# Performance work log

Hardware: AMD Instinct MI355X
Metric: run time of the kernel (lower is better)

The kernel has to match this reference:

```python
import jax, jax.numpy as jnp
import numpy as np
from jax import lax

GAMMA = 1.0
LAM = 1.0
ITERS = 20          # fixed PGD iterations for the graph fused-lasso solve
B = 2048            # number of graphs
NMAX = 1536         # max graph size (for padded per-graph sparsemax)


def setup_inputs() -> dict:
    sizes = (512 + (np.arange(B, dtype=np.int64) * 997) % 1025).astype(np.int32)
    N = int(sizes.sum())  # 2098092
    offsets = np.concatenate([[0], np.cumsum(sizes)[:-1]]).astype(np.int64)
    gid = np.repeat(np.arange(B, dtype=np.int64), sizes)
    # chain edges within each graph
    same = gid[1:] == gid[:-1]
    ca = np.arange(N - 1, dtype=np.int64)[same]
    cb = ca + 1
    # one random intra-graph edge per node
    rng = np.random.RandomState(0)
    u = rng.randint(0, 1 << 30, size=(N, 2)).astype(np.int64)
    ra = offsets[gid] + u[:, 0] % sizes[gid]
    rb = offsets[gid] + u[:, 1] % sizes[gid]
    edges = np.stack([np.concatenate([ca, ra]), np.concatenate([cb, rb])], axis=1).astype(np.int32)
    key = jax.random.key(0)
    x = jax.random.normal(key, (N,), dtype=jnp.float32)
    return {"x": x, "sizes": jnp.asarray(sizes), "edges": jnp.asarray(edges)}


def _gfusedmax(x, sizes, edges):
    N = x.shape[0]
    a = edges[:, 0]
    b = edges[:, 1]
    # --- graph fused lasso: min_y 0.5||y-x||^2 + LAM * sum_e |y_a - y_b|
    # solved on the dual via projected gradient: y = x - D^T u, u in [-LAM, LAM]^E
    deg = jnp.zeros((N,), x.dtype).at[a].add(1.0).at[b].add(1.0)
    step = 1.0 / (2.0 * jnp.max(deg))  # 1/L, L <= 2*max_degree

    def dT(u):  # D^T u : node accumulation of signed edge duals
        return jnp.zeros_like(x).at[a].add(u).at[b].add(-u)

    def body(u, _):
        y = x - dT(u)
        u = jnp.clip(u + step * (y[a] - y[b]), -LAM, LAM)
        return u, None

    u0 = jnp.zeros((a.shape[0],), x.dtype)
    u, _ = lax.scan(body, u0, None, length=ITERS)
    y = x - dT(u)

    # --- per-graph sparsemax(y / GAMMA) over ragged segments, scaled by graph size
    offsets = jnp.concatenate([jnp.zeros((1,), sizes.dtype), jnp.cumsum(sizes)[:-1]])
    gid = jnp.repeat(jnp.arange(B), sizes, total_repeat_length=N)   # [N] graph id
    pos = jnp.arange(N) - offsets[gid]                               # [N] pos in graph
    z = y / GAMMA
    NEG = jnp.asarray(-1e30, z.dtype)
    padded = jnp.full((B, NMAX), NEG, z.dtype).at[gid, pos].set(z)   # [B, NMAX]
    zs = -jnp.sort(-padded, axis=1)                                  # descending
    k = jnp.arange(1, NMAX + 1, dtype=z.dtype)
    cs = jnp.cumsum(zs, axis=1)
    support = (1.0 + k * zs) > cs                                    # padded entries fail
    kmax = jnp.sum(support, axis=1)                                  # [B], >= 1
    cs_k = jnp.take_along_axis(cs, (kmax - 1)[:, None], axis=1)[:, 0]
    tau = (cs_k - 1.0) / kmax.astype(z.dtype)
    p = jnp.maximum(z - tau[gid], 0.0)
    return p * sizes[gid].astype(z.dtype)


def reference(x, sizes, edges):
    return _gfusedmax(x, sizes, edges)
```

## Files before the change

kernel.cpp:

```cpp
#include <hip/hip_runtime.h>

#define NT 512
#define NWAVE 8
#define NTS 256
#define CAP 2064
#define SLOT 5
#define GMAXN 1536
#define TVITERS 20
#define BISECT 14
#define BMAX 4096
#define NBIN 1025

__device__ int g_off[BMAX];
__device__ int g_rank[BMAX];
__device__ int g_maxdeg;

__global__ __launch_bounds__(NTS) void k_scan(const int* __restrict__ sizes, int B) {
  __shared__ int wt[4];
  __shared__ int histC[NBIN];
  __shared__ int histO[NBIN];
  int t = threadIdx.x;
  int lane = t & 63, wid = t >> 6;

  int per = (B + NTS - 1) / NTS;
  int base = t * per;
  int acc = 0;
  for (int k = 0; k < per; ++k) {
    int i = base + k;
    if (i < B) acc += sizes[i];
  }
  int inc = acc;
  #pragma unroll
  for (int o = 1; o < 64; o <<= 1) {
    int n = __shfl_up(inc, o, 64);
    if (lane >= o) inc += n;
  }
  if (lane == 63) wt[wid] = inc;
  __syncthreads();
  int wpre = 0;
  #pragma unroll
  for (int w = 0; w < 4; ++w) wpre += (w < wid) ? wt[w] : 0;
  int run = wpre + inc - acc;
  for (int k = 0; k < per; ++k) {
    int i = base + k;
    if (i < B) { g_off[i] = run; run += sizes[i]; }
  }
  if (t == 0) g_maxdeg = 0;

  for (int i = t; i < NBIN; i += NTS) histC[i] = 0;
  __syncthreads();
  for (int i = t; i < B; i += NTS) atomicAdd(&histC[sizes[i] - 512], 1);
  __syncthreads();
  int c[5];
  int tot = 0;
  #pragma unroll
  for (int k = 0; k < 5; ++k) {
    int i = t * 5 + k;
    int v = (i < NBIN) ? histC[i] : 0;
    c[k] = tot; tot += v;
  }
  inc = tot;
  #pragma unroll
  for (int o = 1; o < 64; o <<= 1) {
    int n = __shfl_up(inc, o, 64);
    if (lane >= o) inc += n;
  }
  if (lane == 63) wt[wid] = inc;
  __syncthreads();
  wpre = 0;
  #pragma unroll
  for (int w = 0; w < 4; ++w) wpre += (w < wid) ? wt[w] : 0;
  int basep = wpre + (inc - tot);
  #pragma unroll
  for (int k = 0; k < 5; ++k) {
    int i = t * 5 + k;
    if (i < NBIN) histO[i] = basep + c[k];
  }
  __syncthreads();
  for (int i = t; i < B; i += NTS) {
    int r = atomicAdd(&histO[sizes[i] - 512], 1);
    g_rank[r] = i;
  }
}

__global__ __launch_bounds__(NTS) void k_deg(const int* __restrict__ sizes,
                                             const int* __restrict__ edges,
                                             int N, int B) {
  __shared__ int cnt[GMAXN];
  __shared__ int wred[4];
  int g = blockIdx.x;
  int t = threadIdx.x;
  int s = sizes[g];
  int off = g_off[g];
  for (int i = t; i < s; i += NTS)
    cnt[i] = 2 - (i == 0 ? 1 : 0) - (i == s - 1 ? 1 : 0);
  __syncthreads();
  const int2* re2 = (const int2*)(edges) + (N - B) + off;
  for (int j = t; j < s; j += NTS) {
    int2 e = re2[j];
    atomicAdd(&cnt[e.x - off], 1);
    atomicAdd(&cnt[e.y - off], 1);
  }
  __syncthreads();
  int m = 0;
  for (int i = t; i < s; i += NTS) m = max(m, cnt[i]);
  #pragma unroll
  for (int o = 32; o > 0; o >>= 1) m = max(m, __shfl_down(m, o, 64));
  if ((t & 63) == 0) wred[t >> 6] = m;
  __syncthreads();
  if (t == 0) {
    m = max(max(wred[0], wred[1]), max(wred[2], wred[3]));
    atomicMax(&g_maxdeg, m);
  }
}

__global__ __launch_bounds__(NT)
void k_main(const float* __restrict__ x,
            const int* __restrict__ sizes,
            const int* __restrict__ edges,
            float* __restrict__ out,
            int N, int B) {
  __shared__ float yL[CAP];
  __shared__ float uE[2 * CAP];
  __shared__ float uCh[CAP];
  __shared__ ushort offL[CAP + 2];
  __shared__ float redf[2][2 * NWAVE];
  __shared__ int wtot[NWAVE];

  int b = blockIdx.x;
  int t = threadIdx.x;
  int lane = t & 63, wid = t >> 6;
  int g1 = g_rank[b];
  int g2i = B - 1 - b;
  int g2 = (g2i != b) ? g_rank[g2i] : -1;
  int s1g = sizes[g1], off1g = g_off[g1];
  int s2g = 0, off2g = 0;
  if (g2 >= 0) { s2g = sizes[g2]; off2g = g_off[g2]; }
  float step = 1.0f / (2.0f * (float)g_maxdeg);
  int nch = N - B;
  int npass = (s1g + s2g <= CAP) ? 1 : 2;

  for (int pass = 0; pass < npass; ++pass) {
    int ss1, oo1, ss2, oo2;
    if (npass == 1) { ss1 = s1g; oo1 = off1g; ss2 = s2g; oo2 = off2g; }
    else { ss1 = pass ? s2g : s1g; oo1 = pass ? off2g : off1g; ss2 = 0; oo2 = 0; }
    int S = ss1 + ss2;
    __syncthreads();

    uint ab[SLOT];
    #pragma unroll
    for (int k = 0; k < SLOT; ++k) {
      int j = t + k * NT;
      uint pk = 0;
      if (j < S) {
        int2 e;
        if (j < ss1) { e = ((const int2*)edges)[nch + oo1 + j];
                       pk = (uint)(e.x - oo1) | ((uint)(e.y - oo1) << 16); }
        else         { e = ((const int2*)edges)[nch + oo2 + (j - ss1)];
                       pk = (uint)(e.x - oo2 + ss1) | ((uint)(e.y - oo2 + ss1) << 16); }
      }
      ab[k] = pk;
    }
    float xr[SLOT];
    #pragma unroll
    for (int k = 0; k < SLOT; ++k) {
      int i = t + k * NT;
      float v = 0.0f;
      if (i < S) v = (i < ss1) ? x[oo1 + i] : x[oo2 + i - ss1];
      xr[k] = v;
    }

    int* cnt = (int*)yL;
    #pragma unroll
    for (int k = 0; k < SLOT; ++k) { int i = t + k * NT; if (i < S) cnt[i] = 0; }
    __syncthreads();
    #pragma unroll
    for (int k = 0; k < SLOT; ++k) {
      int j = t + k * NT;
      if (j < S) {
        atomicAdd(&cnt[ab[k] & 0xFFFFu], 1);
        atomicAdd(&cnt[ab[k] >> 16], 1);
      }
    }
    __syncthreads();
    int c[SLOT];
    int tot = 0;
    #pragma unroll
    for (int k = 0; k < SLOT; ++k) {
      int i = t * SLOT + k;
      int v = (i < S) ? cnt[i] : 0;
      c[k] = tot; tot += v;
    }
    int inc = tot;
    #pragma unroll
    for (int o = 1; o < 64; o <<= 1) {
      int n = __shfl_up(inc, o, 64);
      if (lane >= o) inc += n;
    }
    if (lane == 63) wtot[wid] = inc;
    __syncthreads();
    int wpre = 0;
    #pragma unroll
    for (int w = 0; w < NWAVE; ++w) wpre += (w < wid) ? wtot[w] : 0;
    int basep = wpre + (inc - tot);
    int* cur = (int*)uE;
    #pragma unroll
    for (int k = 0; k < SLOT; ++k) {
      int i = t * SLOT + k;
      if (i < S) { int v = basep + c[k]; offL[i] = (ushort)v; cur[i] = v; }
    }
    if (t == 0) offL[S] = (ushort)(2 * S);
    __syncthreads();
    uint pw[SLOT];
    #pragma unroll
    for (int k = 0; k < SLOT; ++k) {
      int j = t + k * NT;
      uint v = 0;
      if (j < S) {
        int pa = atomicAdd(&cur[ab[k] & 0xFFFFu], 1);
        int pb = atomicAdd(&cur[ab[k] >> 16], 1);
        v = (uint)pa | ((uint)pb << 16);
      }
      pw[k] = v;
    }
    uint pq[SLOT];
    #pragma unroll
    for (int k = 0; k < SLOT; ++k) {
      int i = t + k * NT;
      uint v = 0;
      if (i < S) { uint p0 = offL[i]; uint n = (uint)offL[i + 1] - p0; v = p0 | (n << 16); }
      pq[k] = v;
    }
    float yreg[SLOT], uC[SLOT], uRr[SLOT];
    #pragma unroll
    for (int k = 0; k < SLOT; ++k) {
      int i = t + k * NT;
      uC[k] = 0.0f; uRr[k] = 0.0f;
      if (i < S) { yL[i] = xr[k]; uCh[i] = 0.0f; }
      yreg[k] = (i < S) ? xr[k] : -1e30f;
    }
    __syncthreads();

    for (int it = 0; it < TVITERS; ++it) {
      bool last = (it == TVITERS - 1);
      float yn[SLOT], ya[SLOT], yb[SLOT];
      #pragma unroll
      for (int k = 0; k < SLOT; ++k) {
        int i = t + k * NT;
        yn[k] = (i + 1 < S) ? yL[i + 1] : 0.0f;
      }
      #pragma unroll
      for (int k = 0; k < SLOT; ++k) {
        int j = t + k * NT;
        if (j < S) {
          ya[k] = yL[ab[k] & 0xFFFFu];
          yb[k] = yL[ab[k] >> 16];
        }
      }
      #pragma unroll
      for (int k = 0; k < SLOT; ++k) {
        int i = t + k * NT;
        bool ch = (i < S - 1) && (i != ss1 - 1);
        if (ch) {
          float nu = uC[k] + step * (yreg[k] - yn[k]);
          nu = fminf(1.0f, fmaxf(-1.0f, nu));
          uC[k] = nu;
          uCh[i] = nu;
        }
      }
      #pragma unroll
      for (int k = 0; k < SLOT; ++k) {
        int j = t + k * NT;
        if (j < S) {
          float nu = uRr[k] + step * (ya[k] - yb[k]);
          nu = fminf(1.0f, fmaxf(-1.0f, nu));
          uRr[k] = nu;
          uE[pw[k] & 0xFFFFu] = -nu;
          uE[pw[k] >> 16] = nu;
        }
      }
      __syncthreads();
      #pragma unroll
      for (int k = 0; k < SLOT; ++k) {
        int i = t + k * NT;
        if (i < S) {
          float y = xr[k];
          if (i > 0 && i != ss1) y += uCh[i - 1];
          if ((i < S - 1) && (i != ss1 - 1)) y -= uC[k];
          uint p = pq[k] & 0xFFFFu, n = pq[k] >> 16;
          for (uint q = 0; q < n; ++q) y += uE[p + q];
          yreg[k] = y;
          if (!last) yL[i] = y;
        }
      }
      if (!last) __syncthreads();
    }

    float m1 = -1e30f, m2 = -1e30f;
    #pragma unroll
    for (int k = 0; k < SLOT; ++k) {
      int i = t + k * NT;
      if (i < S) { if (i < ss1) m1 = fmaxf(m1, yreg[k]); else m2 = fmaxf(m2, yreg[k]); }
    }
    #pragma unroll
    for (int o = 1; o < 64; o <<= 1) {
      m1 = fmaxf(m1, __shfl_xor(m1, o, 64));
      m2 = fmaxf(m2, __shfl_xor(m2, o, 64));
    }
    if (lane == 0) { redf[0][wid] = m1; redf[0][NWAVE + wid] = m2; }
    __syncthreads();
    m1 = -1e30f; m2 = -1e30f;
    #pragma unroll
    for (int w = 0; w < NWAVE; ++w) {
      m1 = fmaxf(m1, redf[0][w]);
      m2 = fmaxf(m2, redf[0][NWAVE + w]);
    }

    float lo1 = m1 - 1.0f, hi1 = m1, lo2 = m2 - 1.0f, hi2 = m2;
    int par = 1;
    for (int r = 0; r < BISECT; ++r) {
      float mid1 = 0.5f * (lo1 + hi1), mid2 = 0.5f * (lo2 + hi2);
      float f1 = 0.0f, f2 = 0.0f;
      #pragma unroll
      for (int k = 0; k < SLOT; ++k) {
        int i = t + k * NT;
        if (i < S) {
          if (i < ss1) f1 += fmaxf(yreg[k] - mid1, 0.0f);
          else         f2 += fmaxf(yreg[k] - mid2, 0.0f);
        }
      }
      #pragma unroll
      for (int o = 1; o < 64; o <<= 1) {
        f1 += __shfl_xor(f1, o, 64);
        f2 += __shfl_xor(f2, o, 64);
      }
      if (lane == 0) { redf[par][wid] = f1; redf[par][NWAVE + wid] = f2; }
      __syncthreads();
      f1 = 0.0f; f2 = 0.0f;
      #pragma unroll
      for (int w = 0; w < NWAVE; ++w) {
        f1 += redf[par][w];
        f2 += redf[par][NWAVE + w];
      }
      par ^= 1;
      if (f1 >= 1.0f) lo1 = mid1; else hi1 = mid1;
      if (f2 >= 1.0f) lo2 = mid2; else hi2 = mid2;
    }
    __syncthreads();
    float cf1 = 0.0f, S1 = 0.0f, cf2 = 0.0f, S2 = 0.0f;
    #pragma unroll
    for (int k = 0; k < SLOT; ++k) {
      int i = t + k * NT;
      if (i < S) {
        if (i < ss1) { if (yreg[k] > lo1) { cf1 += 1.0f; S1 += yreg[k]; } }
        else         { if (yreg[k] > lo2) { cf2 += 1.0f; S2 += yreg[k]; } }
      }
    }
    #pragma unroll
    for (int o = 1; o < 64; o <<= 1) {
      cf1 += __shfl_xor(cf1, o, 64);
      S1  += __shfl_xor(S1,  o, 64);
      cf2 += __shfl_xor(cf2, o, 64);
      S2  += __shfl_xor(S2,  o, 64);
    }
    float* redflat = (float*)redf;
    if (lane == 0) {
      redflat[wid] = cf1; redflat[NWAVE + wid] = S1;
      redflat[2 * NWAVE + wid] = cf2; redflat[3 * NWAVE + wid] = S2;
    }
    __syncthreads();
    cf1 = 0.0f; S1 = 0.0f; cf2 = 0.0f; S2 = 0.0f;
    #pragma unroll
    for (int w = 0; w < NWAVE; ++w) {
      cf1 += redflat[w];
      S1  += redflat[NWAVE + w];
      cf2 += redflat[2 * NWAVE + w];
      S2  += redflat[3 * NWAVE + w];
    }
    float tau1 = (S1 - 1.0f) / cf1;
    float tau2 = (cf2 > 0.0f) ? (S2 - 1.0f) / cf2 : 0.0f;

    float sf1 = (float)ss1, sf2 = (float)ss2;
    #pragma unroll
    for (int k = 0; k < SLOT; ++k) {
      int i = t + k * NT;
      if (i < S) {
        bool in2 = (i >= ss1);
        float tau = in2 ? tau2 : tau1;
        float sf = in2 ? sf2 : sf1;
        int o = in2 ? (oo2 + i - ss1) : (oo1 + i);
        out[o] = fmaxf(yreg[k] - tau, 0.0f) * sf;
      }
    }
  }
}

extern "C" void kernel_launch(void* const* d_in, const int* in_sizes, int n_in,
                              void* d_out, int out_size, void* d_ws, size_t ws_size,
                              hipStream_t stream) {
  const float* x = (const float*)d_in[0];
  const int* sizes = (const int*)d_in[1];
  const int* edges = (const int*)d_in[2];
  float* out = (float*)d_out;
  int N = in_sizes[0];
  int B = in_sizes[1];
  (void)d_ws; (void)ws_size; (void)n_in; (void)out_size;

  k_scan<<<1, NTS, 0, stream>>>(sizes, B);
  k_deg<<<B, NTS, 0, stream>>>(sizes, edges, N, B);
  int nb = (B + 1) / 2;
  k_main<<<nb, NT, 0, stream>>>(x, sizes, edges, out, N, B);
}
```

Before: 182.3 us.

## Switch to blocked per-thread node layout and pass chain duals via shuffles

Each thread now owns a contiguous run of SLOT nodes (i0 = t*SLOT) instead of a strided set, so chain-edge neighbours sit mostly in registers. Chain duals cross thread boundaries through __shfl_up and a small per-wave LDS array, which removes the uCh shared array and the per-iteration neighbour loads. CSR offsets and degrees are kept in registers instead of the offL array, and CAP/SLOT drop to 2048/4, cutting LDS and register use. Blocked indexing makes global loads and stores less coalesced, and pairs whose combined size exceeds 2048 now need two passes.

```diff
diff --git a/kernel.cpp b/kernel.cpp
--- a/kernel.cpp
+++ b/kernel.cpp
@@ -3,8 +3,8 @@
 #define NT 512
 #define NWAVE 8
 #define NTS 256
-#define CAP 2064
-#define SLOT 5
+#define CAP 2048
+#define SLOT 4
 #define GMAXN 1536
 #define TVITERS 20
 #define BISECT 14
@@ -122,8 +122,7 @@
             int N, int B) {
   __shared__ float yL[CAP];
   __shared__ float uE[2 * CAP];
-  __shared__ float uCh[CAP];
-  __shared__ ushort offL[CAP + 2];
+  __shared__ float uBc[NWAVE];
   __shared__ float redf[2][2 * NWAVE];
   __shared__ int wtot[NWAVE];
 
@@ -145,12 +144,13 @@
     if (npass == 1) { ss1 = s1g; oo1 = off1g; ss2 = s2g; oo2 = off2g; }
     else { ss1 = pass ? s2g : s1g; oo1 = pass ? off2g : off1g; ss2 = 0; oo2 = 0; }
     int S = ss1 + ss2;
+    int i0 = t * SLOT;
     __syncthreads();
 
     uint ab[SLOT];
     #pragma unroll
     for (int k = 0; k < SLOT; ++k) {
-      int j = t + k * NT;
+      int j = i0 + k;
       uint pk = 0;
       if (j < S) {
         int2 e;
@@ -164,7 +164,7 @@
     float xr[SLOT];
     #pragma unroll
     for (int k = 0; k < SLOT; ++k) {
-      int i = t + k * NT;
+      int i = i0 + k;
       float v = 0.0f;
       if (i < S) v = (i < ss1) ? x[oo1 + i] : x[oo2 + i - ss1];
       xr[k] = v;
@@ -172,24 +172,24 @@
 
     int* cnt = (int*)yL;
     #pragma unroll
-    for (int k = 0; k < SLOT; ++k) { int i = t + k * NT; if (i < S) cnt[i] = 0; }
-    __syncthreads();
-    #pragma unroll
-    for (int k = 0; k < SLOT; ++k) {
-      int j = t + k * NT;
+    for (int k = 0; k < SLOT; ++k) { int i = i0 + k; if (i < S) cnt[i] = 0; }
+    __syncthreads();
+    #pragma unroll
+    for (int k = 0; k < SLOT; ++k) {
+      int j = i0 + k;
       if (j < S) {
         atomicAdd(&cnt[ab[k] & 0xFFFFu], 1);
         atomicAdd(&cnt[ab[k] >> 16], 1);
       }
     }
     __syncthreads();
-    int c[SLOT];
+    int cex[SLOT], deg[SLOT];
     int tot = 0;
     #pragma unroll
     for (int k = 0; k < SLOT; ++k) {
-      int i = t * SLOT + k;
+      int i = i0 + k;
       int v = (i < S) ? cnt[i] : 0;
-      c[k] = tot; tot += v;
+      cex[k] = tot; tot += v; deg[k] = v;
     }
     int inc = tot;
     #pragma unroll
@@ -204,17 +204,19 @@
     for (int w = 0; w < NWAVE; ++w) wpre += (w < wid) ? wtot[w] : 0;
     int basep = wpre + (inc - tot);
     int* cur = (int*)uE;
-    #pragma unroll
-    for (int k = 0; k < SLOT; ++k) {
-      int i = t * SLOT + k;
-      if (i < S) { int v = basep + c[k]; offL[i] = (ushort)v; cur[i] = v; }
-    }
-    if (t == 0) offL[S] = (ushort)(2 * S);
+    uint pq[SLOT];
+    #pragma unroll
+    for (int k = 0; k < SLOT; ++k) {
+      int i = i0 + k;
+      int p0 = basep + cex[k];
+      pq[k] = (uint)p0 | ((uint)deg[k] << 16);
+      if (i < S) cur[i] = p0;
+    }
     __syncthreads();
     uint pw[SLOT];
     #pragma unroll
     for (int k = 0; k < SLOT; ++k) {
-      int j = t + k * NT;
+      int j = i0 + k;
       uint v = 0;
       if (j < S) {
         int pa = atomicAdd(&cur[ab[k] & 0xFFFFu], 1);
@@ -223,54 +225,42 @@
       }
       pw[k] = v;
     }
-    uint pq[SLOT];
-    #pragma unroll
-    for (int k = 0; k < SLOT; ++k) {
-      int i = t + k * NT;
-      uint v = 0;
-      if (i < S) { uint p0 = offL[i]; uint n = (uint)offL[i + 1] - p0; v = p0 | (n << 16); }
-      pq[k] = v;
-    }
+    __syncthreads();
     float yreg[SLOT], uC[SLOT], uRr[SLOT];
     #pragma unroll
     for (int k = 0; k < SLOT; ++k) {
-      int i = t + k * NT;
+      int i = i0 + k;
       uC[k] = 0.0f; uRr[k] = 0.0f;
-      if (i < S) { yL[i] = xr[k]; uCh[i] = 0.0f; }
+      if (i < S) yL[i] = xr[k];
       yreg[k] = (i < S) ? xr[k] : -1e30f;
     }
     __syncthreads();
 
     for (int it = 0; it < TVITERS; ++it) {
       bool last = (it == TVITERS - 1);
-      float yn[SLOT], ya[SLOT], yb[SLOT];
+      float ya[SLOT], yb[SLOT];
       #pragma unroll
       for (int k = 0; k < SLOT; ++k) {
-        int i = t + k * NT;
-        yn[k] = (i + 1 < S) ? yL[i + 1] : 0.0f;
-      }
-      #pragma unroll
-      for (int k = 0; k < SLOT; ++k) {
-        int j = t + k * NT;
+        int j = i0 + k;
         if (j < S) {
           ya[k] = yL[ab[k] & 0xFFFFu];
           yb[k] = yL[ab[k] >> 16];
         }
       }
+      float ylast = ((i0 + SLOT) < S) ? yL[i0 + SLOT] : 0.0f;
       #pragma unroll
       for (int k = 0; k < SLOT; ++k) {
-        int i = t + k * NT;
-        bool ch = (i < S - 1) && (i != ss1 - 1);
-        if (ch) {
-          float nu = uC[k] + step * (yreg[k] - yn[k]);
-          nu = fminf(1.0f, fmaxf(-1.0f, nu));
-          uC[k] = nu;
-          uCh[i] = nu;
+        int i = i0 + k;
+        if ((i + 1 < S) && (i + 1 != ss1)) {
+          float ynx = (k < SLOT - 1) ? yreg[k + 1] : ylast;
+          float nu = uC[k] + step * (yreg[k] - ynx);
+          uC[k] = fminf(1.0f, fmaxf(-1.0f, nu));
         }
       }
+      if (lane == 63) uBc[wid] = uC[SLOT - 1];
       #pragma unroll
       for (int k = 0; k < SLOT; ++k) {
-        int j = t + k * NT;
+        int j = i0 + k;
         if (j < S) {
           float nu = uRr[k] + step * (ya[k] - yb[k]);
           nu = fminf(1.0f, fmaxf(-1.0f, nu));
@@ -280,13 +270,16 @@
         }
       }
       __syncthreads();
+      float upPrev = __shfl_up(uC[SLOT - 1], 1, 64);
+      if (lane == 0) upPrev = (wid > 0) ? uBc[wid - 1] : 0.0f;
       #pragma unroll
       for (int k = 0; k < SLOT; ++k) {
-        int i = t + k * NT;
+        int i = i0 + k;
         if (i < S) {
           float y = xr[k];
-          if (i > 0 && i != ss1) y += uCh[i - 1];
-          if ((i < S - 1) && (i != ss1 - 1)) y -= uC[k];
+          float cl = (k == 0) ? upPrev : uC[k - 1];
+          if (i > 0 && i != ss1) y += cl;
+          if ((i + 1 < S) && (i + 1 != ss1)) y -= uC[k];
           uint p = pq[k] & 0xFFFFu, n = pq[k] >> 16;
           for (uint q = 0; q < n; ++q) y += uE[p + q];
           yreg[k] = y;
@@ -299,7 +292,7 @@
     float m1 = -1e30f, m2 = -1e30f;
     #pragma unroll
     for (int k = 0; k < SLOT; ++k) {
-      int i = t + k * NT;
+      int i = i0 + k;
       if (i < S) { if (i < ss1) m1 = fmaxf(m1, yreg[k]); else m2 = fmaxf(m2, yreg[k]); }
     }
     #pragma unroll
@@ -323,7 +316,7 @@
       float f1 = 0.0f, f2 = 0.0f;
       #pragma unroll
       for (int k = 0; k < SLOT; ++k) {
-        int i = t + k * NT;
+        int i = i0 + k;
         if (i < S) {
           if (i < ss1) f1 += fmaxf(yreg[k] - mid1, 0.0f);
           else         f2 += fmaxf(yreg[k] - mid2, 0.0f);
@@ -350,7 +343,7 @@
     float cf1 = 0.0f, S1 = 0.0f, cf2 = 0.0f, S2 = 0.0f;
     #pragma unroll
     for (int k = 0; k < SLOT; ++k) {
-      int i = t + k * NT;
+      int i = i0 + k;
       if (i < S) {
         if (i < ss1) { if (yreg[k] > lo1) { cf1 += 1.0f; S1 += yreg[k]; } }
         else         { if (yreg[k] > lo2) { cf2 += 1.0f; S2 += yreg[k]; } }
@@ -383,7 +376,7 @@
     float sf1 = (float)ss1, sf2 = (float)ss2;
     #pragma unroll
     for (int k = 0; k < SLOT; ++k) {
-      int i = t + k * NT;
+      int i = i0 + k;
       if (i < S) {
         bool in2 = (i >= ss1);
         float tau = in2 ? tau2 : tau1;
```

After: 258.6 us. 1.42x slower.

## Replace CSR edge gather with LDS float atomics and double-buffered y

Applied to the files above, without the earlier changes.

Drops the per-pass CSR build (count, prefix scan, slot assignment) used to gather edge duals per node. Instead, each iteration writes y from chain duals into a second LDS buffer, then scatters random-edge duals into it with shared-memory float atomicAdd, swapping buffers between iterations. Chain neighbour values now come from wave shuffles, with a fallback for lane 63. This removes the setup atomics and scans but adds two LDS atomics per edge per iteration, an extra barrier per iteration, and makes float summation order nondeterministic.

```diff
diff --git a/kernel.cpp b/kernel.cpp
--- a/kernel.cpp
+++ b/kernel.cpp
@@ -120,12 +120,9 @@
             const int* __restrict__ edges,
             float* __restrict__ out,
             int N, int B) {
-  __shared__ float yL[CAP];
-  __shared__ float uE[2 * CAP];
-  __shared__ float uCh[CAP];
-  __shared__ ushort offL[CAP + 2];
+  __shared__ float yA[CAP];
+  __shared__ float yB[CAP];
   __shared__ float redf[2][2 * NWAVE];
-  __shared__ int wtot[NWAVE];
 
   int b = blockIdx.x;
   int t = threadIdx.x;
@@ -168,104 +165,39 @@
       float v = 0.0f;
       if (i < S) v = (i < ss1) ? x[oo1 + i] : x[oo2 + i - ss1];
       xr[k] = v;
-    }
-
-    int* cnt = (int*)yL;
-    #pragma unroll
-    for (int k = 0; k < SLOT; ++k) { int i = t + k * NT; if (i < S) cnt[i] = 0; }
-    __syncthreads();
-    #pragma unroll
-    for (int k = 0; k < SLOT; ++k) {
-      int j = t + k * NT;
-      if (j < S) {
-        atomicAdd(&cnt[ab[k] & 0xFFFFu], 1);
-        atomicAdd(&cnt[ab[k] >> 16], 1);
-      }
-    }
-    __syncthreads();
-    int c[SLOT];
-    int tot = 0;
-    #pragma unroll
-    for (int k = 0; k < SLOT; ++k) {
-      int i = t * SLOT + k;
-      int v = (i < S) ? cnt[i] : 0;
-      c[k] = tot; tot += v;
-    }
-    int inc = tot;
-    #pragma unroll
-    for (int o = 1; o < 64; o <<= 1) {
-      int n = __shfl_up(inc, o, 64);
-      if (lane >= o) inc += n;
-    }
-    if (lane == 63) wtot[wid] = inc;
-    __syncthreads();
-    int wpre = 0;
-    #pragma unroll
-    for (int w = 0; w < NWAVE; ++w) wpre += (w < wid) ? wtot[w] : 0;
-    int basep = wpre + (inc - tot);
-    int* cur = (int*)uE;
-    #pragma unroll
-    for (int k = 0; k < SLOT; ++k) {
-      int i = t * SLOT + k;
-      if (i < S) { int v = basep + c[k]; offL[i] = (ushort)v; cur[i] = v; }
-    }
-    if (t == 0) offL[S] = (ushort)(2 * S);
-    __syncthreads();
-    uint pw[SLOT];
-    #pragma unroll
-    for (int k = 0; k < SLOT; ++k) {
-      int j = t + k * NT;
-      uint v = 0;
-      if (j < S) {
-        int pa = atomicAdd(&cur[ab[k] & 0xFFFFu], 1);
-        int pb = atomicAdd(&cur[ab[k] >> 16], 1);
-        v = (uint)pa | ((uint)pb << 16);
-      }
-      pw[k] = v;
-    }
-    uint pq[SLOT];
-    #pragma unroll
-    for (int k = 0; k < SLOT; ++k) {
-      int i = t + k * NT;
-      uint v = 0;
-      if (i < S) { uint p0 = offL[i]; uint n = (uint)offL[i + 1] - p0; v = p0 | (n << 16); }
-      pq[k] = v;
-    }
-    float yreg[SLOT], uC[SLOT], uRr[SLOT];
-    #pragma unroll
-    for (int k = 0; k < SLOT; ++k) {
-      int i = t + k * NT;
-      uC[k] = 0.0f; uRr[k] = 0.0f;
-      if (i < S) { yL[i] = xr[k]; uCh[i] = 0.0f; }
-      yreg[k] = (i < S) ? xr[k] : -1e30f;
-    }
-    __syncthreads();
-
+      if (i < S) yA[i] = v;
+    }
+    float uC[SLOT], uRr[SLOT];
+    #pragma unroll
+    for (int k = 0; k < SLOT; ++k) { uC[k] = 0.0f; uRr[k] = 0.0f; }
+    __syncthreads();
+
+    float* yIn = yA;
+    float* yOut = yB;
     for (int it = 0; it < TVITERS; ++it) {
-      bool last = (it == TVITERS - 1);
-      float yn[SLOT], ya[SLOT], yb[SLOT];
+      float yi[SLOT], ya[SLOT], yb[SLOT];
       #pragma unroll
       for (int k = 0; k < SLOT; ++k) {
         int i = t + k * NT;
-        yn[k] = (i + 1 < S) ? yL[i + 1] : 0.0f;
+        yi[k] = (i < S) ? yIn[i] : 0.0f;
       }
       #pragma unroll
       for (int k = 0; k < SLOT; ++k) {
         int j = t + k * NT;
         if (j < S) {
-          ya[k] = yL[ab[k] & 0xFFFFu];
-          yb[k] = yL[ab[k] >> 16];
+          ya[k] = yIn[ab[k] & 0xFFFFu];
+          yb[k] = yIn[ab[k] >> 16];
         }
       }
       #pragma unroll
       for (int k = 0; k < SLOT; ++k) {
         int i = t + k * NT;
-        bool ch = (i < S - 1) && (i != ss1 - 1);
-        if (ch) {
-          float nu = uC[k] + step * (yreg[k] - yn[k]);
-          nu = fminf(1.0f, fmaxf(-1.0f, nu));
-          uC[k] = nu;
-          uCh[i] = nu;
+        float ynx = __shfl_down(yi[k], 1, 64);
+        if (lane == 63 && i + 1 < S) ynx = yIn[i + 1];
+        bool hasR = (i + 1 < S) && (i + 1 != ss1);
+        if (hasR) {
+          float nu = uC[k] + step * (yi[k] - ynx);
+          uC[k] = fminf(1.0f, fmaxf(-1.0f, nu));
         }
       }
       #pragma unroll
@@ -273,27 +205,45 @@
         int j = t + k * NT;
         if (j < S) {
           float nu = uRr[k] + step * (ya[k] - yb[k]);
-          nu = fminf(1.0f, fmaxf(-1.0f, nu));
-          uRr[k] = nu;
-          uE[pw[k] & 0xFFFFu] = -nu;
-          uE[pw[k] >> 16] = nu;
-        }
-      }
-      __syncthreads();
+          uRr[k] = fminf(1.0f, fmaxf(-1.0f, nu));
+        }
+      }
       #pragma unroll
       for (int k = 0; k < SLOT; ++k) {
         int i = t + k * NT;
+        float upL = __shfl_up(uC[k], 1, 64);
         if (i < S) {
           float y = xr[k];
-          if (i > 0 && i != ss1) y += uCh[i - 1];
-          if ((i < S - 1) && (i != ss1 - 1)) y -= uC[k];
-          uint p = pq[k] & 0xFFFFu, n = pq[k] >> 16;
-          for (uint q = 0; q < n; ++q) y += uE[p + q];
-          yreg[k] = y;
-          if (!last) yL[i] = y;
-        }
-      }
-      if (!last) __syncthreads();
+          if (lane > 0 && i > 0 && i != ss1) y += upL;
+          if ((i + 1 < S) && (i + 1 != ss1)) y -= uC[k];
+          yOut[i] = y;
+        }
+      }
+      __syncthreads();
+      if (lane == 63) {
+        #pragma unroll
+        for (int k = 0; k < SLOT; ++k) {
+          int i = t + k * NT;
+          if ((i + 1 < S) && (i + 1 != ss1)) atomicAdd(&yOut[i + 1], uC[k]);
+        }
+      }
+      #pragma unroll
+      for (int k = 0; k < SLOT; ++k) {
+        int j = t + k * NT;
+        if (j < S) {
+          atomicAdd(&yOut[ab[k] & 0xFFFFu], -uRr[k]);
+          atomicAdd(&yOut[ab[k] >> 16], uRr[k]);
+        }
+      }
+      __syncthreads();
+      float* tmp = yIn; yIn = yOut; yOut = tmp;
+    }
+
+    float yreg[SLOT];
+    #pragma unroll
+    for (int k = 0; k < SLOT; ++k) {
+      int i = t + k * NT;
+      yreg[k] = (i < S) ? yIn[i] : -1e30f;
     }
 
     float m1 = -1e30f, m2 = -1e30f;
```

Measured after the change: 540.7 us. 197% more time.

## Fuse scan into degree kernel and pass chain duals via wave shuffles

Applied to the files above, without the earlier changes.

Removes the single-block scan kernel. Each degree block now computes its own graph offset by summing the preceding sizes, block 0 builds the size-rank ordering, and per-graph max degrees are written to an array that every main block reduces. In the TV iteration, chain-edge dual values and neighbour y values are exchanged with wave shuffles plus a small per-wave boundary buffer instead of the uCh shared array and extra LDS reads. This saves one launch and some LDS traffic, but each pre block does redundant O(B) prefix work and each main block does an O(B) max reduction.

```diff
diff --git a/kernel.cpp b/kernel.cpp
--- a/kernel.cpp
+++ b/kernel.cpp
@@ -2,7 +2,7 @@
 
 #define NT 512
 #define NWAVE 8
-#define NTS 256
+#define NTP 256
 #define CAP 2064
 #define SLOT 5
 #define GMAXN 1536
@@ -13,104 +13,90 @@
 
 __device__ int g_off[BMAX];
 __device__ int g_rank[BMAX];
-__device__ int g_maxdeg;
-
-__global__ __launch_bounds__(NTS) void k_scan(const int* __restrict__ sizes, int B) {
-  __shared__ int wt[4];
-  __shared__ int histC[NBIN];
-  __shared__ int histO[NBIN];
-  int t = threadIdx.x;
-  int lane = t & 63, wid = t >> 6;
-
-  int per = (B + NTS - 1) / NTS;
-  int base = t * per;
-  int acc = 0;
-  for (int k = 0; k < per; ++k) {
-    int i = base + k;
-    if (i < B) acc += sizes[i];
-  }
-  int inc = acc;
-  #pragma unroll
-  for (int o = 1; o < 64; o <<= 1) {
-    int n = __shfl_up(inc, o, 64);
-    if (lane >= o) inc += n;
-  }
-  if (lane == 63) wt[wid] = inc;
-  __syncthreads();
-  int wpre = 0;
-  #pragma unroll
-  for (int w = 0; w < 4; ++w) wpre += (w < wid) ? wt[w] : 0;
-  int run = wpre + inc - acc;
-  for (int k = 0; k < per; ++k) {
-    int i = base + k;
-    if (i < B) { g_off[i] = run; run += sizes[i]; }
-  }
-  if (t == 0) g_maxdeg = 0;
-
-  for (int i = t; i < NBIN; i += NTS) histC[i] = 0;
-  __syncthreads();
-  for (int i = t; i < B; i += NTS) atomicAdd(&histC[sizes[i] - 512], 1);
-  __syncthreads();
-  int c[5];
-  int tot = 0;
-  #pragma unroll
-  for (int k = 0; k < 5; ++k) {
-    int i = t * 5 + k;
-    int v = (i < NBIN) ? histC[i] : 0;
-    c[k] = tot; tot += v;
-  }
-  inc = tot;
-  #pragma unroll
-  for (int o = 1; o < 64; o <<= 1) {
-    int n = __shfl_up(inc, o, 64);
-    if (lane >= o) inc += n;
-  }
-  if (lane == 63) wt[wid] = inc;
-  __syncthreads();
-  wpre = 0;
-  #pragma unroll
-  for (int w = 0; w < 4; ++w) wpre += (w < wid) ? wt[w] : 0;
-  int basep = wpre + (inc - tot);
-  #pragma unroll
-  for (int k = 0; k < 5; ++k) {
-    int i = t * 5 + k;
-    if (i < NBIN) histO[i] = basep + c[k];
-  }
-  __syncthreads();
-  for (int i = t; i < B; i += NTS) {
-    int r = atomicAdd(&histO[sizes[i] - 512], 1);
-    g_rank[r] = i;
-  }
-}
-
-__global__ __launch_bounds__(NTS) void k_deg(const int* __restrict__ sizes,
+__device__ int g_degmax[BMAX];
+
+__global__ __launch_bounds__(NTP) void k_pre(const int* __restrict__ sizes,
                                              const int* __restrict__ edges,
                                              int N, int B) {
   __shared__ int cnt[GMAXN];
-  __shared__ int wred[4];
+  __shared__ int histO[NBIN];
+  __shared__ int red[4];
   int g = blockIdx.x;
   int t = threadIdx.x;
+  int lane = t & 63, wid = t >> 6;
+
+  int acc = 0;
+  for (int i = t; i < g; i += NTP) acc += sizes[i];
+  #pragma unroll
+  for (int o = 1; o < 64; o <<= 1) acc += __shfl_xor(acc, o, 64);
+  if (lane == 0) red[wid] = acc;
+  __syncthreads();
+  int off = (red[0] + red[1]) + (red[2] + red[3]);
   int s = sizes[g];
-  int off = g_off[g];
-  for (int i = t; i < s; i += NTS)
-    cnt[i] = 2 - (i == 0 ? 1 : 0) - (i == s - 1 ? 1 : 0);
-  __syncthreads();
-  const int2* re2 = (const int2*)(edges) + (N - B) + off;
-  for (int j = t; j < s; j += NTS) {
+  if (t == 0) g_off[g] = off;
+  __syncthreads();
+
+  for (int i = t; i < s; i += NTP) cnt[i] = 0;
+  __syncthreads();
+  const int2* re2 = (const int2*)edges + (N - B) + off;
+  for (int j = t; j < s; j += NTP) {
     int2 e = re2[j];
     atomicAdd(&cnt[e.x - off], 1);
     atomicAdd(&cnt[e.y - off], 1);
   }
   __syncthreads();
   int m = 0;
-  for (int i = t; i < s; i += NTS) m = max(m, cnt[i]);
+  for (int i = t; i < s; i += NTP) {
+    int chain = 2 - (i == 0 ? 1 : 0) - (i == s - 1 ? 1 : 0);
+    m = max(m, cnt[i] + chain);
+  }
   #pragma unroll
-  for (int o = 32; o > 0; o >>= 1) m = max(m, __shfl_down(m, o, 64));
-  if ((t & 63) == 0) wred[t >> 6] = m;
+  for (int o = 1; o < 64; o <<= 1) m = max(m, __shfl_xor(m, o, 64));
+  if (lane == 0) red[wid] = m;
   __syncthreads();
   if (t == 0) {
-    m = max(max(wred[0], wred[1]), max(wred[2], wred[3]));
-    atomicMax(&g_maxdeg, m);
+    m = max(max(red[0], red[1]), max(red[2], red[3]));
+    g_degmax[g] = m;
+  }
+
+  if (g == 0) {
+    int* histC = cnt;
+    __syncthreads();
+    for (int i = t; i < NBIN; i += NTP) histC[i] = 0;
+    __syncthreads();
+    for (int i = t; i < B; i += NTP) atomicAdd(&histC[sizes[i] - 512], 1);
+    __syncthreads();
+    int c[5];
+    int tot = 0;
+    #pragma unroll
+    for (int k = 0; k < 5; ++k) {
+      int i = t * 5 + k;
+      int v = (i < NBIN) ? histC[i] : 0;
+      c[k] = tot; tot += v;
+    }
+    int inc = tot;
+    #pragma unroll
+    for (int o = 1; o < 64; o <<= 1) {
+      int n = __shfl_up(inc, o, 64);
+      if (lane >= o) inc += n;
+    }
+    __syncthreads();
+    if (lane == 63) red[wid] = inc;
+    __syncthreads();
+    int wpre = 0;
+    #pragma unroll
+    for (int w = 0; w < 4; ++w) wpre += (w < wid) ? red[w] : 0;
+    int basep = wpre + (inc - tot);
+    #pragma unroll
+    for (int k = 0; k < 5; ++k) {
+      int i = t * 5 + k;
+      if (i < NBIN) histO[i] = basep + c[k];
+    }
+    __syncthreads();
+    for (int i = t; i < B; i += NTP) {
+      int r = atomicAdd(&histO[sizes[i] - 512], 1);
+      g_rank[r] = i;
+    }
   }
 }
 
@@ -122,21 +108,33 @@
             int N, int B) {
   __shared__ float yL[CAP];
   __shared__ float uE[2 * CAP];
-  __shared__ float uCh[CAP];
   __shared__ ushort offL[CAP + 2];
+  __shared__ float uB[NWAVE][SLOT];
   __shared__ float redf[2][2 * NWAVE];
   __shared__ int wtot[NWAVE];
+  __shared__ int mdred[NWAVE];
 
   int b = blockIdx.x;
   int t = threadIdx.x;
   int lane = t & 63, wid = t >> 6;
+
+  int md = 0;
+  for (int i = t; i < B; i += NT) md = max(md, g_degmax[i]);
+  #pragma unroll
+  for (int o = 1; o < 64; o <<= 1) md = max(md, __shfl_xor(md, o, 64));
+  if (lane == 0) mdred[wid] = md;
+  __syncthreads();
+  md = 0;
+  #pragma unroll
+  for (int w = 0; w < NWAVE; ++w) md = max(md, mdred[w]);
+  float step = 1.0f / (2.0f * (float)md);
+
   int g1 = g_rank[b];
   int g2i = B - 1 - b;
   int g2 = (g2i != b) ? g_rank[g2i] : -1;
   int s1g = sizes[g1], off1g = g_off[g1];
   int s2g = 0, off2g = 0;
   if (g2 >= 0) { s2g = sizes[g2]; off2g = g_off[g2]; }
-  float step = 1.0f / (2.0f * (float)g_maxdeg);
   int nch = N - B;
   int npass = (s1g + s2g <= CAP) ? 1 : 2;
 
@@ -236,19 +234,14 @@
     for (int k = 0; k < SLOT; ++k) {
       int i = t + k * NT;
       uC[k] = 0.0f; uRr[k] = 0.0f;
-      if (i < S) { yL[i] = xr[k]; uCh[i] = 0.0f; }
+      if (i < S) yL[i] = xr[k];
       yreg[k] = (i < S) ? xr[k] : -1e30f;
     }
     __syncthreads();
 
     for (int it = 0; it < TVITERS; ++it) {
       bool last = (it == TVITERS - 1);
-      float yn[SLOT], ya[SLOT], yb[SLOT];
-      #pragma unroll
-      for (int k = 0; k < SLOT; ++k) {
-        int i = t + k * NT;
-        yn[k] = (i + 1 < S) ? yL[i + 1] : 0.0f;
-      }
+      float ya[SLOT], yb[SLOT];
       #pragma unroll
       for (int k = 0; k < SLOT; ++k) {
         int j = t + k * NT;
@@ -260,13 +253,16 @@
       #pragma unroll
       for (int k = 0; k < SLOT; ++k) {
         int i = t + k * NT;
-        bool ch = (i < S - 1) && (i != ss1 - 1);
-        if (ch) {
-          float nu = uC[k] + step * (yreg[k] - yn[k]);
-          nu = fminf(1.0f, fmaxf(-1.0f, nu));
-          uC[k] = nu;
-          uCh[i] = nu;
+        float ynx = __shfl_down(yreg[k], 1, 64);
+        if (lane == 63 && i + 1 < S) ynx = yL[i + 1];
+        if ((i + 1 < S) && (i + 1 != ss1)) {
+          float nu = uC[k] + step * (yreg[k] - ynx);
+          uC[k] = fminf(1.0f, fmaxf(-1.0f, nu));
         }
+      }
+      if (lane == 63) {
+        #pragma unroll
+        for (int k = 0; k < SLOT; ++k) uB[wid][k] = uC[k];
       }
       #pragma unroll
       for (int k = 0; k < SLOT; ++k) {
@@ -282,11 +278,14 @@
       __syncthreads();
       #pragma unroll
       for (int k = 0; k < SLOT; ++k) {
+        float upL = __shfl_up(uC[k], 1, 64);
+        if (lane == 0)
+          upL = (wid > 0) ? uB[wid - 1][k] : ((k > 0) ? uB[NWAVE - 1][k - 1] : 0.0f);
         int i = t + k * NT;
         if (i < S) {
           float y = xr[k];
-          if (i > 0 && i != ss1) y += uCh[i - 1];
-          if ((i < S - 1) && (i != ss1 - 1)) y -= uC[k];
+          if (i > 0 && i != ss1) y += upL;
+          if ((i + 1 < S) && (i + 1 != ss1)) y -= uC[k];
           uint p = pq[k] & 0xFFFFu, n = pq[k] >> 16;
           for (uint q = 0; q < n; ++q) y += uE[p + q];
           yreg[k] = y;
@@ -406,8 +405,7 @@
   int B = in_sizes[1];
   (void)d_ws; (void)ws_size; (void)n_in; (void)out_size;
 
-  k_scan<<<1, NTS, 0, stream>>>(sizes, B);
-  k_deg<<<B, NTS, 0, stream>>>(sizes, edges, N, B);
+  k_pre<<<B, NTP, 0, stream>>>(sizes, edges, N, B);
   int nb = (B + 1) / 2;
   k_main<<<nb, NT, 0, stream>>>(x, sizes, edges, out, N, B);
 }
```

After: 171.5 us. -5.9%, faster.
